# Kernel tuning notes

Hardware: AMD Instinct MI355X
Metric: run time of the kernel (lower is better)

## Reference

```python
import jax, jax.numpy as jnp
import numpy as np

B, S, D = 30, 1024, 128      # batch (hardcoded by module), seq_len, input_dim
ET, H, NH = 128, 4, 128      # embed_time, num_heads, nhidden
DK = ET // H


def setup_inputs() -> dict:
    key = jax.random.key(0)
    ks = jax.random.split(key, 32)
    s = 0.05
    p = lambda i, shape: jax.random.normal(ks[i], shape, jnp.float32) * s
    return dict(
        x=jax.random.normal(ks[0], (B, S, D), jnp.float32),
        time_steps=jax.random.uniform(ks[1], (B, S), jnp.float32),
        # learned time embedding: Linear(1,1) and Linear(1, ET-1)
        w_lin=p(2, (1, 1)), b_lin=p(3, (1,)),
        w_per=p(4, (ET - 1, 1)), b_per=p(5, (ET - 1,)),
        # attention projections
        Wq=p(6, (ET, ET)), bq=p(7, (ET,)),
        Wk=p(8, (ET, ET)), bk=p(9, (ET,)),
        Wo=p(10, (NH, D * H)), bo=p(11, (NH,)),
        # bidirectional GRU (forward / backward directions)
        Wih_f=p(12, (3 * NH, NH)), Whh_f=p(13, (3 * NH, NH)),
        bih_f=p(14, (3 * NH,)), bhh_f=p(15, (3 * NH,)),
        Wih_b=p(16, (3 * NH, NH)), Whh_b=p(17, (3 * NH, NH)),
        bih_b=p(18, (3 * NH,)), bhh_b=p(19, (3 * NH,)),
        # classifier (no activations in original Sequential)
        W1=p(20, (128, 2 * NH)), b1=p(21, (128,)),
        W2=p(22, (64, 128)), b2=p(23, (64,)),
        W3=p(24, (6, 64)), b3=p(25, (6,)),
    )


def _gru_final(xseq, Wih, Whh, bih, bhh):
    # xseq: [S, B, NH]; returns final hidden [B, NH] (PyTorch GRU equations)
    def step(h, xt):
        gi = xt @ Wih.T + bih
        gh = h @ Whh.T + bhh
        ir, iz, inn = jnp.split(gi, 3, axis=-1)
        hr, hz, hn = jnp.split(gh, 3, axis=-1)
        r = jax.nn.sigmoid(ir + hr)
        z = jax.nn.sigmoid(iz + hz)
        n = jnp.tanh(inn + r * hn)
        h_new = (1.0 - z) * n + z * h
        return h_new, None
    h0 = jnp.zeros((xseq.shape[1], Whh.shape[1]), xseq.dtype)
    hT, _ = jax.lax.scan(step, h0, xseq)
    return hT


def reference(x, time_steps, w_lin, b_lin, w_per, b_per, Wq, bq, Wk, bk, Wo, bo,
              Wih_f, Whh_f, bih_f, bhh_f, Wih_b, Whh_b, bih_b, bhh_b,
              W1, b1, W2, b2, W3, b3):
    # learned time embedding: cat([Linear(1,1)(t), sin(Linear(1,ET-1)(t))], -1)
    tt = time_steps[..., None]                                   # [B,S,1]
    te = jnp.concatenate([tt @ w_lin.T + b_lin,
                          jnp.sin(tt @ w_per.T + b_per)], -1)    # [B,S,ET]
    # q/k projections, split into heads
    q = (te @ Wq.T + bq).reshape(B, S, H, DK).transpose(0, 2, 1, 3)  # [B,H,S,DK]
    k = (te @ Wk.T + bk).reshape(B, S, H, DK).transpose(0, 2, 1, 3)
    scores = jnp.einsum('bhqd,bhkd->bhqk', q, k) / jnp.sqrt(jnp.float32(DK))
    # mask=None, dropout=None => the repeat_interleave over the feature dim is
    # redundant: softmax over the key axis is identical for every feature, so
    # sum(p_attn * value) == softmax(scores) @ value exactly.
    attn = jax.nn.softmax(scores, axis=-1)                       # [B,H,S,S]
    ctx = jnp.einsum('bhqk,bkd->bhqd', attn, x)                  # [B,H,S,D]
    att_out = ctx.transpose(0, 2, 1, 3).reshape(B, S, H * D) @ Wo.T + bo  # [B,S,NH]
    # bidirectional GRU; only final hidden states are used downstream
    xs = att_out.transpose(1, 0, 2)                              # [S,B,NH]
    hf = _gru_final(xs, Wih_f, Whh_f, bih_f, bhh_f)
    hb = _gru_final(xs[::-1], Wih_b, Whh_b, bih_b, bhh_b)
    cin = jnp.concatenate([hf, hb], axis=-1)                     # [B,2*NH]
    h1 = cin @ W1.T + b1
    h2 = h1 @ W2.T + b2
    return h2 @ W3.T + b3                                        # [B,6]
```

## Files before the change

### kernel.cpp

```cpp
#include <hip/hip_runtime.h>
#include <math.h>

#define B_ 30
#define S_ 1024
#define D_ 128
#define ET_ 128
#define H_ 4
#define DK_ 32
#define NH_ 128
#define NPOS (B_*S_)

#define OFF_TE   0L
#define OFF_Q    3932160L
#define OFF_K    7864320L
#define OFF_CTX  11796480L
#define OFF_XS   0L
#define OFF_GIF  3932160L
#define OFF_GIB  15728640L
#define OFF_HF   27525120L
#define OFF_HB   27528960L

typedef __attribute__((ext_vector_type(4))) short short4v;
typedef __attribute__((ext_vector_type(8))) short short8v;
typedef __attribute__((ext_vector_type(4))) float f32x4;

__device__ __forceinline__ short f2bf(float x) {
    unsigned u = __builtin_bit_cast(unsigned, x);
    unsigned r = (u + 0x7FFFu + ((u >> 16) & 1u)) >> 16;
    return (short)r;
}
__device__ __forceinline__ float bf2f(short s) {
    unsigned u = ((unsigned)(unsigned short)s) << 16;
    return __builtin_bit_cast(float, u);
}

__device__ __forceinline__ short8v pack8(const float4 a, const float4 b) {
    short8v v;
    v[0]=f2bf(a.x); v[1]=f2bf(a.y); v[2]=f2bf(a.z); v[3]=f2bf(a.w);
    v[4]=f2bf(b.x); v[5]=f2bf(b.y); v[6]=f2bf(b.z); v[7]=f2bf(b.w);
    return v;
}

__device__ __forceinline__ void pack_hilo(const float4 a, const float4 b,
                                          short8v& hi, short8v& lo) {
    float v[8] = {a.x,a.y,a.z,a.w,b.x,b.y,b.z,b.w};
#pragma unroll
    for (int e = 0; e < 8; ++e) {
        hi[e] = f2bf(v[e]);
        lo[e] = f2bf(v[e] - bf2f(hi[e]));
    }
}

__device__ __forceinline__ float fsigmoid(float x) {
    return __builtin_amdgcn_rcpf(1.f + __expf(-x));
}
__device__ __forceinline__ float ftanh(float x) {
    return 1.f - 2.f * __builtin_amdgcn_rcpf(__expf(2.f * x) + 1.f);
}

__device__ __forceinline__ void sync_lds() {
    asm volatile("s_waitcnt lgkmcnt(0)" ::: "memory");
    __builtin_amdgcn_sched_barrier(0);
    __builtin_amdgcn_s_barrier();
    __builtin_amdgcn_sched_barrier(0);
}

__global__ __launch_bounds__(256) void time_embed_kernel(
    const float* __restrict__ ts, const float* __restrict__ w_lin,
    const float* __restrict__ b_lin, const float* __restrict__ w_per,
    const float* __restrict__ b_per, float* __restrict__ te)
{
    const long idx = (long)blockIdx.x * 256 + threadIdx.x;
    const int pos = (int)(idx >> 7);
    const int j = (int)(idx & 127);
    const float tv = ts[pos];
    float v;
    if (j == 0) v = tv * w_lin[0] + b_lin[0];
    else        v = sinf(tv * w_per[j-1] + b_per[j-1]);
    te[idx] = v;
}

template<int REMAP, int FOLD>
__global__ __launch_bounds__(256) void gemm_mfma_kernel(
    const float* __restrict__ A, const float* __restrict__ W,
    const float* __restrict__ bias, const float* __restrict__ bias2,
    float* __restrict__ C, int M, int N, int K)
{
    __shared__ short A_hi[64][72], A_lo[64][72];
    __shared__ short W_hi[128][72], W_lo[128][72];
    const int t = threadIdx.x;
    const int m0 = blockIdx.x * 64;
    const int n0 = blockIdx.y * 128;
    const int w = t >> 6, lane = t & 63;
    const int l15 = lane & 15, lg = lane >> 4;

    f32x4 acc[8];
#pragma unroll
    for (int i = 0; i < 8; ++i) acc[i] = (f32x4){0.f,0.f,0.f,0.f};

    for (int k0 = 0; k0 < K; k0 += 64) {
        {
            const int r = t >> 2, c16 = (t & 3) * 16;
            const int m = m0 + r;
            long src;
            if (REMAP == 2) {
                const int s = m / B_, bb = m % B_;
                src = (long)((S_-1-s)*B_ + bb) * K;
            } else {
                src = (long)m * K;
            }
            const float4* ap = (const float4*)(A + src + k0 + c16);
            short8v h0, l0, h1, l1;
            pack_hilo(ap[0], ap[1], h0, l0);
            pack_hilo(ap[2], ap[3], h1, l1);
            *(short8v*)&A_hi[r][c16]     = h0;
            *(short8v*)&A_hi[r][c16 + 8] = h1;
            *(short8v*)&A_lo[r][c16]     = l0;
            *(short8v*)&A_lo[r][c16 + 8] = l1;
        }
        {
            const int n = t >> 1, c32 = (t & 1) * 32;
            const float4* wp = (const float4*)(W + (long)(n0 + n) * K + k0 + c32);
#pragma unroll
            for (int q = 0; q < 4; ++q) {
                short8v h, l;
                pack_hilo(wp[2*q], wp[2*q + 1], h, l);
                *(short8v*)&W_hi[n][c32 + 8*q] = h;
                *(short8v*)&W_lo[n][c32 + 8*q] = l;
            }
        }
        __syncthreads();
#pragma unroll
        for (int kk = 0; kk < 64; kk += 32) {
            short8v ah = *(const short8v*)&A_hi[16*w + l15][kk + 8*lg];
            short8v al = *(const short8v*)&A_lo[16*w + l15][kk + 8*lg];
#pragma unroll
            for (int nf = 0; nf < 8; ++nf) {
                short8v wh = *(const short8v*)&W_hi[16*nf + l15][kk + 8*lg];
                short8v wl = *(const short8v*)&W_lo[16*nf + l15][kk + 8*lg];
                acc[nf] = __builtin_amdgcn_mfma_f32_16x16x32_bf16(ah, wh, acc[nf], 0,0,0);
                acc[nf] = __builtin_amdgcn_mfma_f32_16x16x32_bf16(al, wh, acc[nf], 0,0,0);
                acc[nf] = __builtin_amdgcn_mfma_f32_16x16x32_bf16(ah, wl, acc[nf], 0,0,0);
            }
        }
        __syncthreads();
    }

#pragma unroll
    for (int nf = 0; nf < 8; ++nf) {
#pragma unroll
        for (int r = 0; r < 4; ++r) {
            const int n = n0 + 16*nf + l15;
            const int m = m0 + 16*w + 4*lg + r;
            float v = acc[nf][r] + bias[n];
            if (FOLD) { if (n < 256) v += bias2[n]; }
            if (REMAP == 1) {
                const int bb = m / S_, s = m % S_;
                C[(long)(s*B_ + bb) * N + n] = v;
            } else {
                C[(long)m * N + n] = v;
            }
        }
    }
}

#define SCALE_LOG2 (0.17677669529663687f * 1.4426950408889634f)

__global__ __launch_bounds__(256) void attn_kernel(
    const float* __restrict__ qbuf, const float* __restrict__ kbuf,
    const float* __restrict__ x, float* __restrict__ ctx)
{
    const int qt = blockIdx.x;
    const int h  = blockIdx.y;
    const int b  = blockIdx.z;
    const int q0 = qt * 64;
    const int t  = threadIdx.x;
    const int w    = t >> 6;
    const int lane = t & 63;
    const int l15  = lane & 15;
    const int lg   = lane >> 4;

    __shared__ short K_lds[64][40];
    __shared__ short XT_lds[128][68];
    __shared__ short P_lds[4][16][88];

    short8v qf;
    {
        const float* qp = qbuf + ((long)(b*S_ + q0 + 16*w + l15))*ET_ + h*DK_ + 8*lg;
        float4 a = *(const float4*)qp;
        float4 c = *(const float4*)(qp + 4);
        a.x*=SCALE_LOG2; a.y*=SCALE_LOG2; a.z*=SCALE_LOG2; a.w*=SCALE_LOG2;
        c.x*=SCALE_LOG2; c.y*=SCALE_LOG2; c.z*=SCALE_LOG2; c.w*=SCALE_LOG2;
        qf = pack8(a, c);
    }

    short8v ones;
#pragma unroll
    for (int i = 0; i < 8; ++i) ones[i] = (short)0x3F80;

    f32x4 acc[8];
#pragma unroll
    for (int i = 0; i < 8; ++i) acc[i] = (f32x4){0.f,0.f,0.f,0.f};
    float lsum = 0.f;
    const f32x4 zf = (f32x4){0.f,0.f,0.f,0.f};

    for (int kt = 0; kt < 16; ++kt) {
        const int key0 = kt * 64;
        {
            const int key = t >> 2, c8 = (t & 3) * 8;
            const float* kp = kbuf + ((long)(b*S_ + key0 + key))*ET_ + h*DK_ + c8;
            float4 a = *(const float4*)kp;
            float4 c = *(const float4*)(kp + 4);
            *(short8v*)&K_lds[key][c8] = pack8(a, c);
        }
        {
            const int k2 = t & 31;
            const int dg = t >> 5;
            const float* xp0 = x + ((long)(b*S_ + key0 + 2*k2))*D_ + 16*dg;
            const float* xp1 = xp0 + D_;
            float v0[16], v1[16];
#pragma unroll
            for (int j4 = 0; j4 < 4; ++j4) {
                float4 a = ((const float4*)xp0)[j4];
                float4 c = ((const float4*)xp1)[j4];
                v0[4*j4+0]=a.x; v0[4*j4+1]=a.y; v0[4*j4+2]=a.z; v0[4*j4+3]=a.w;
                v1[4*j4+0]=c.x; v1[4*j4+1]=c.y; v1[4*j4+2]=c.z; v1[4*j4+3]=c.w;
            }
#pragma unroll
            for (int j = 0; j < 16; ++j) {
                unsigned u = (unsigned)(unsigned short)f2bf(v0[j])
                           | ((unsigned)(unsigned short)f2bf(v1[j]) << 16);
                *(unsigned*)&XT_lds[16*dg + j][2*k2] = u;
            }
        }
        __syncthreads();

        f32x4 sc[4];
#pragma unroll
        for (int f = 0; f < 4; ++f) {
            short8v kf = *(const short8v*)&K_lds[16*f + l15][8*lg];
            sc[f] = __builtin_amdgcn_mfma_f32_16x16x32_bf16(kf, qf, zf, 0, 0, 0);
        }

        float pw[4][4];
        float ps = 0.f;
#pragma unroll
        for (int f = 0; f < 4; ++f)
#pragma unroll
            for (int r = 0; r < 4; ++r) {
                const float p = exp2f(sc[f][r]);
                ps += p;
                pw[f][r] = p - 1.f;
            }
        ps += __shfl_xor(ps, 16);
        ps += __shfl_xor(ps, 32);
        lsum += ps;

#pragma unroll
        for (int f = 0; f < 4; ++f) {
            unsigned lo = (unsigned)(unsigned short)f2bf(pw[f][0])
                        | ((unsigned)(unsigned short)f2bf(pw[f][1]) << 16);
            unsigned hi = (unsigned)(unsigned short)f2bf(pw[f][2])
                        | ((unsigned)(unsigned short)f2bf(pw[f][3]) << 16);
            *(unsigned*)&P_lds[w][l15][16*f + 4*lg]     = lo;
            *(unsigned*)&P_lds[w][l15][16*f + 4*lg + 2] = hi;
        }

#pragma unroll
        for (int kb = 0; kb < 2; ++kb) {
            short8v pa = *(const short8v*)&P_lds[w][l15][32*kb + 8*lg];
#pragma unroll
            for (int dq = 0; dq < 8; ++dq) {
                const short* xr = &XT_lds[16*dq + l15][32*kb + 8*lg];
                short4v lo = *(const short4v*)xr;
                short4v hi = *(const short4v*)(xr + 4);
                short8v xb = __builtin_shufflevector(lo, hi, 0,1,2,3,4,5,6,7);
                acc[dq] = __builtin_amdgcn_mfma_f32_16x16x32_bf16(ones, xb, acc[dq], 0, 0, 0);
                acc[dq] = __builtin_amdgcn_mfma_f32_16x16x32_bf16(pa,   xb, acc[dq], 0, 0, 0);
            }
        }
        __syncthreads();
    }

    const float inv = 1.f / lsum;
#pragma unroll
    for (int r = 0; r < 4; ++r) {
        const float ir = __shfl(inv, (lane & 48) | (4*lg + r));
        const long base = ((long)(b*S_ + q0 + 16*w + 4*lg + r)*H_ + h)*D_ + l15;
#pragma unroll
        for (int d = 0; d < 8; ++d)
            ctx[base + (long)d*16] = acc[d][r] * ir;
    }
}

__global__ __launch_bounds__(512, 1) void gru_kernel(
    const float* __restrict__ gi_f, const float* __restrict__ gi_b,
    const float* __restrict__ Whh_f, const float* __restrict__ bhh_f,
    const float* __restrict__ Whh_b, const float* __restrict__ bhh_b,
    float* __restrict__ hf, float* __restrict__ hb)
{
    const int bid = blockIdx.x;
    const int dir = bid / B_;
    const int b   = bid % B_;
    const float* gi  = dir ? gi_b  : gi_f;
    const float* Whh = dir ? Whh_b : Whh_f;
    const float* bhh = dir ? bhh_b : bhh_f;
    float* hout      = dir ? hb    : hf;
    const int t    = threadIdx.x;
    const int w    = t >> 6;
    const int lane = t & 63;
    const int l15  = lane & 15;
    const int lg   = lane >> 4;
    const int sel  = l15 >> 3;

    short8v wa[3][4];
#pragma unroll
    for (int rt = 0; rt < 3; ++rt) {
        const int row = (3*w + rt)*16 + l15;
#pragma unroll
        for (int kf = 0; kf < 4; ++kf) {
            const float* wp = Whh + (long)row*128 + 32*kf + 8*lg;
            float4 a = *(const float4*)wp;
            float4 c = *(const float4*)(wp + 4);
            wa[rt][kf] = pack8(a, c);
        }
    }

    __shared__ __align__(16) float ghs[800];
    __shared__ __align__(16) short hbf[2][2][160];

    float hreg = 0.f;
    float bnj = 0.f;
    float gar = 0.f, gaz = 0.f, gan = 0.f;
    float gbr = 0.f, gbz = 0.f, gbn = 0.f;
    float gcr = 0.f, gcz = 0.f, gcn = 0.f;
    float gdr = 0.f, gdz = 0.f, gdn = 0.f;
    if (t < 128) {
        hbf[0][0][t] = 0; hbf[0][1][t] = 0;
        bnj = bhh[256 + t];
        const float* g0 = gi + (long)b * 384;
        gar = g0[t]; gaz = g0[128+t]; gan = g0[256+t];
        const float* g1 = gi + ((long)B_ + b) * 384;
        gbr = g1[t]; gbz = g1[128+t]; gbn = g1[256+t];
    }
    __syncthreads();

#define LOADGI(R, Z, N, SS)                                                    \
    if (t < 128 && (SS) < S_) {                                                \
        const float* g = gi + ((long)(SS)*B_ + b) * 384;                       \
        R = g[t]; Z = g[128+t]; N = g[256+t];                                  \
    }

#define GRU_STEP(CUR, GR, GZ, GN)                                              \
    {                                                                          \
        short8v hfrag[4];                                                      \
        _Pragma("unroll")                                                      \
        for (int kf = 0; kf < 4; ++kf)                                         \
            hfrag[kf] = *(const short8v*)&hbf[CUR][sel][32*kf + 8*lg];         \
        _Pragma("unroll")                                                      \
        for (int rt = 0; rt < 3; ++rt) {                                       \
            f32x4 cacc = (f32x4){0.f,0.f,0.f,0.f};                             \
            _Pragma("unroll")                                                  \
            for (int kf = 0; kf < 4; ++kf)                                     \
                cacc = __builtin_amdgcn_mfma_f32_16x16x32_bf16(                \
                    wa[rt][kf], hfrag[kf], cacc, 0,0,0);                       \
            if (l15 == 0)                                                      \
                *(f32x4*)&ghs[(3*w + rt)*16 + 4*lg] = cacc;                    \
            else if (l15 == 8)                                                 \
                *(f32x4*)&ghs[400 + (3*w + rt)*16 + 4*lg] = cacc;              \
        }                                                                      \
        sync_lds();                                                            \
        if (t < 128) {                                                         \
            const float ghr = ghs[t]       + ghs[400+t];                       \
            const float ghz = ghs[128+t]   + ghs[528+t];                       \
            const float ghn = ghs[256+t]   + ghs[656+t];                       \
            const float r = fsigmoid(GR + ghr);                                \
            const float z = fsigmoid(GZ + ghz);                                \
            const float n = ftanh (GN + r * (ghn + bnj));                      \
            hreg = (1.f - z)*n + z*hreg;                                       \
            const short hi = f2bf(hreg);                                       \
            hbf[(CUR)^1][0][t] = hi;                                           \
            hbf[(CUR)^1][1][t] = f2bf(hreg - bf2f(hi));                        \
        }                                                                      \
        sync_lds();                                                            \
    }

    for (int s = 0; s < S_; s += 4) {
        LOADGI(gcr, gcz, gcn, s + 2)
        GRU_STEP(0, gar, gaz, gan)
        LOADGI(gdr, gdz, gdn, s + 3)
        GRU_STEP(1, gbr, gbz, gbn)
        LOADGI(gar, gaz, gan, s + 4)
        GRU_STEP(0, gcr, gcz, gcn)
        LOADGI(gbr, gbz, gbn, s + 5)
        GRU_STEP(1, gdr, gdz, gdn)
    }
#undef GRU_STEP
#undef LOADGI

    if (t < 128) hout[(long)b*128 + t] = hreg;
}

__global__ __launch_bounds__(128) void classifier_kernel(
    const float* __restrict__ hf, const float* __restrict__ hb,
    const float* __restrict__ W1, const float* __restrict__ b1,
    const float* __restrict__ W2, const float* __restrict__ b2,
    const float* __restrict__ W3, const float* __restrict__ b3,
    float* __restrict__ out)
{
    const int b = blockIdx.x;
    const int t = threadIdx.x;
    __shared__ float cin[256], a1[128], a2[64];
    cin[t]       = hf[(long)b*128 + t];
    cin[128 + t] = hb[(long)b*128 + t];
    __syncthreads();
    {
        float a = b1[t];
        for (int i = 0; i < 256; ++i) a = fmaf(W1[(long)t*256 + i], cin[i], a);
        a1[t] = a;
    }
    __syncthreads();
    if (t < 64) {
        float a = b2[t];
        for (int i = 0; i < 128; ++i) a = fmaf(W2[(long)t*128 + i], a1[i], a);
        a2[t] = a;
    }
    __syncthreads();
    if (t < 6) {
        float a = b3[t];
        for (int i = 0; i < 64; ++i) a = fmaf(W3[(long)t*64 + i], a2[i], a);
        out[(long)b*6 + t] = a;
    }
}

extern "C" void kernel_launch(void* const* d_in, const int* in_sizes, int n_in,
                              void* d_out, int out_size, void* d_ws, size_t ws_size,
                              hipStream_t stream)
{
    const float* x     = (const float*)d_in[0];
    const float* ts    = (const float*)d_in[1];
    const float* w_lin = (const float*)d_in[2];
    const float* b_lin = (const float*)d_in[3];
    const float* w_per = (const float*)d_in[4];
    const float* b_per = (const float*)d_in[5];
    const float* Wq    = (const float*)d_in[6];
    const float* bq    = (const float*)d_in[7];
    const float* Wk    = (const float*)d_in[8];
    const float* bk    = (const float*)d_in[9];
    const float* Wo    = (const float*)d_in[10];
    const float* bo    = (const float*)d_in[11];
    const float* Wih_f = (const float*)d_in[12];
    const float* Whh_f = (const float*)d_in[13];
    const float* bih_f = (const float*)d_in[14];
    const float* bhh_f = (const float*)d_in[15];
    const float* Wih_b = (const float*)d_in[16];
    const float* Whh_b = (const float*)d_in[17];
    const float* bih_b = (const float*)d_in[18];
    const float* bhh_b = (const float*)d_in[19];
    const float* W1    = (const float*)d_in[20];
    const float* b1    = (const float*)d_in[21];
    const float* W2    = (const float*)d_in[22];
    const float* b2    = (const float*)d_in[23];
    const float* W3    = (const float*)d_in[24];
    const float* b3    = (const float*)d_in[25];
    float* out = (float*)d_out;
    float* ws  = (float*)d_ws;

    float* te  = ws + OFF_TE;
    float* q   = ws + OFF_Q;
    float* k   = ws + OFF_K;
    float* ctx = ws + OFF_CTX;
    float* xs  = ws + OFF_XS;
    float* gif = ws + OFF_GIF;
    float* gib = ws + OFF_GIB;
    float* hf  = ws + OFF_HF;
    float* hb  = ws + OFF_HB;

    time_embed_kernel<<<NPOS*128/256, 256, 0, stream>>>(ts, w_lin, b_lin, w_per, b_per, te);
    gemm_mfma_kernel<0,0><<<dim3(NPOS/64, 1), 256, 0, stream>>>(te, Wq, bq, nullptr, q, NPOS, 128, 128);
    gemm_mfma_kernel<0,0><<<dim3(NPOS/64, 1), 256, 0, stream>>>(te, Wk, bk, nullptr, k, NPOS, 128, 128);
    attn_kernel<<<dim3(16, 4, 30), 256, 0, stream>>>(q, k, x, ctx);
    gemm_mfma_kernel<1,0><<<dim3(NPOS/64, 1), 256, 0, stream>>>(ctx, Wo, bo, nullptr, xs, NPOS, 128, 512);
    gemm_mfma_kernel<0,1><<<dim3(NPOS/64, 3), 256, 0, stream>>>(xs, Wih_f, bih_f, bhh_f, gif, NPOS, 384, 128);
    gemm_mfma_kernel<2,1><<<dim3(NPOS/64, 3), 256, 0, stream>>>(xs, Wih_b, bih_b, bhh_b, gib, NPOS, 384, 128);
    gru_kernel<<<60, 512, 0, stream>>>(gif, gib, Whh_f, bhh_f, Whh_b, bhh_b, hf, hb);
    classifier_kernel<<<30, 128, 0, stream>>>(hf, hb, W1, b1, W2, b2, W3, b3, out);
}
```

Before: 952.7 us.

## Restructure GRU recurrence to two waves with in-register gate extraction

```diff
diff --git a/kernel.cpp b/kernel.cpp
--- a/kernel.cpp
+++ b/kernel.cpp
@@ -293,7 +293,7 @@
     }
 }
 
-__global__ __launch_bounds__(512, 1) void gru_kernel(
+__global__ __launch_bounds__(128, 1) void gru_kernel(
     const float* __restrict__ gi_f, const float* __restrict__ gi_b,
     const float* __restrict__ Whh_f, const float* __restrict__ bhh_f,
     const float* __restrict__ Whh_b, const float* __restrict__ bhh_b,
@@ -307,48 +307,48 @@
     const float* bhh = dir ? bhh_b : bhh_f;
     float* hout      = dir ? hb    : hf;
     const int t    = threadIdx.x;
-    const int w    = t >> 6;
+    const int wv   = t >> 6;
     const int lane = t & 63;
     const int l15  = lane & 15;
     const int lg   = lane >> 4;
-    const int sel  = l15 >> 3;
-
-    short8v wa[3][4];
-#pragma unroll
-    for (int rt = 0; rt < 3; ++rt) {
-        const int row = (3*w + rt)*16 + l15;
-#pragma unroll
-        for (int kf = 0; kf < 4; ++kf) {
-            const float* wp = Whh + (long)row*128 + 32*kf + 8*lg;
-            float4 a = *(const float4*)wp;
-            float4 c = *(const float4*)(wp + 4);
-            wa[rt][kf] = pack8(a, c);
-        }
-    }
-
-    __shared__ __align__(16) float ghs[800];
-    __shared__ __align__(16) short hbf[2][2][160];
-
-    float hreg = 0.f;
-    float bnj = 0.f;
-    float gar = 0.f, gaz = 0.f, gan = 0.f;
-    float gbr = 0.f, gbz = 0.f, gbn = 0.f;
-    float gcr = 0.f, gcz = 0.f, gcn = 0.f;
-    float gdr = 0.f, gdz = 0.f, gdn = 0.f;
-    if (t < 128) {
-        hbf[0][0][t] = 0; hbf[0][1][t] = 0;
-        bnj = bhh[256 + t];
+    const int j    = 64*wv + 16*(l15 >> 2) + 4*lg + (l15 & 3);
+
+    short8v wa[3][4][4];
+#pragma unroll
+    for (int g = 0; g < 3; ++g)
+#pragma unroll
+        for (int A = 0; A < 4; ++A) {
+            const int row = 128*g + 64*wv + 16*A + l15;
+#pragma unroll
+            for (int kf = 0; kf < 4; ++kf) {
+                const float* wp = Whh + (long)row*128 + 32*kf + 8*lg;
+                float4 a = *(const float4*)wp;
+                float4 c = *(const float4*)(wp + 4);
+                wa[g][A][kf] = pack8(a, c);
+            }
+        }
+
+    const float bnj = bhh[256 + j];
+
+    __shared__ __align__(16) short hbf[2][128];
+    hbf[0][t] = 0;
+
+    float hcur = 0.f;
+
+    float gar=0.f, gaz=0.f, gan=0.f, gbr=0.f, gbz=0.f, gbn=0.f;
+    float gcr=0.f, gcz=0.f, gcn=0.f, gdr=0.f, gdz=0.f, gdn=0.f;
+    {
         const float* g0 = gi + (long)b * 384;
-        gar = g0[t]; gaz = g0[128+t]; gan = g0[256+t];
+        gar = g0[j]; gaz = g0[128+j]; gan = g0[256+j];
         const float* g1 = gi + ((long)B_ + b) * 384;
-        gbr = g1[t]; gbz = g1[128+t]; gbn = g1[256+t];
+        gbr = g1[j]; gbz = g1[128+j]; gbn = g1[256+j];
     }
     __syncthreads();
 
 #define LOADGI(R, Z, N, SS)                                                    \
-    if (t < 128 && (SS) < S_) {                                                \
+    if ((SS) < S_) {                                                           \
         const float* g = gi + ((long)(SS)*B_ + b) * 384;                       \
-        R = g[t]; Z = g[128+t]; N = g[256+t];                                  \
+        R = g[j]; Z = g[128+j]; N = g[256+j];                                  \
     }
 
 #define GRU_STEP(CUR, GR, GZ, GN)                                              \
@@ -356,32 +356,39 @@
         short8v hfrag[4];                                                      \
         _Pragma("unroll")                                                      \
         for (int kf = 0; kf < 4; ++kf)                                         \
-            hfrag[kf] = *(const short8v*)&hbf[CUR][sel][32*kf + 8*lg];         \
+            hfrag[kf] = *(const short8v*)&hbf[CUR][32*kf + 8*lg];              \
+        f32x4 acc[3][4];                                                       \
         _Pragma("unroll")                                                      \
-        for (int rt = 0; rt < 3; ++rt) {                                       \
-            f32x4 cacc = (f32x4){0.f,0.f,0.f,0.f};                             \
+        for (int g = 0; g < 3; ++g)                                            \
             _Pragma("unroll")                                                  \
-            for (int kf = 0; kf < 4; ++kf)                                     \
-                cacc = __builtin_amdgcn_mfma_f32_16x16x32_bf16(                \
-                    wa[rt][kf], hfrag[kf], cacc, 0,0,0);                       \
-            if (l15 == 0)                                                      \
-                *(f32x4*)&ghs[(3*w + rt)*16 + 4*lg] = cacc;                    \
-            else if (l15 == 8)                                                 \
-                *(f32x4*)&ghs[400 + (3*w + rt)*16 + 4*lg] = cacc;              \
-        }                                                                      \
-        sync_lds();                                                            \
-        if (t < 128) {                                                         \
-            const float ghr = ghs[t]       + ghs[400+t];                       \
-            const float ghz = ghs[128+t]   + ghs[528+t];                       \
-            const float ghn = ghs[256+t]   + ghs[656+t];                       \
-            const float r = fsigmoid(GR + ghr);                                \
-            const float z = fsigmoid(GZ + ghz);                                \
-            const float n = ftanh (GN + r * (ghn + bnj));                      \
-            hreg = (1.f - z)*n + z*hreg;                                       \
-            const short hi = f2bf(hreg);                                       \
-            hbf[(CUR)^1][0][t] = hi;                                           \
-            hbf[(CUR)^1][1][t] = f2bf(hreg - bf2f(hi));                        \
-        }                                                                      \
+            for (int A = 0; A < 4; ++A)                                        \
+                acc[g][A] = (f32x4){0.f,0.f,0.f,0.f};                          \
+        _Pragma("unroll")                                                      \
+        for (int kf = 0; kf < 4; ++kf)                                         \
+            _Pragma("unroll")                                                  \
+            for (int g = 0; g < 3; ++g)                                        \
+                _Pragma("unroll")                                              \
+                for (int A = 0; A < 4; ++A)                                    \
+                    acc[g][A] = __builtin_amdgcn_mfma_f32_16x16x32_bf16(       \
+                        wa[g][A][kf], hfrag[kf], acc[g][A], 0,0,0);            \
+        float ghr = acc[0][0][0];                                              \
+        float ghz = acc[1][0][0];                                              \
+        float ghn = acc[2][0][0];                                              \
+        _Pragma("unroll")                                                      \
+        for (int A = 0; A < 4; ++A)                                            \
+            _Pragma("unroll")                                                  \
+            for (int R = 0; R < 4; ++R) {                                      \
+                if (A == 0 && R == 0) continue;                                \
+                const bool c = (l15 == 4*A + R);                               \
+                ghr = c ? acc[0][A][R] : ghr;                                  \
+                ghz = c ? acc[1][A][R] : ghz;                                  \
+                ghn = c ? acc[2][A][R] : ghn;                                  \
+            }                                                                  \
+        const float r = fsigmoid(GR + ghr);                                    \
+        const float z = fsigmoid(GZ + ghz);                                    \
+        const float n = ftanh (GN + r * (ghn + bnj));                          \
+        hcur = (1.f - z)*n + z*hcur;                                           \
+        hbf[(CUR)^1][j] = f2bf(hcur);                                          \
         sync_lds();                                                            \
     }
 
@@ -398,7 +405,7 @@
 #undef GRU_STEP
 #undef LOADGI
 
-    if (t < 128) hout[(long)b*128 + t] = hreg;
+    hout[(long)b*128 + j] = hcur;
 }
 
 __global__ __launch_bounds__(128) void classifier_kernel(
@@ -483,6 +490,6 @@
     gemm_mfma_kernel<1,0><<<dim3(NPOS/64, 1), 256, 0, stream>>>(ctx, Wo, bo, nullptr, xs, NPOS, 128, 512);
     gemm_mfma_kernel<0,1><<<dim3(NPOS/64, 3), 256, 0, stream>>>(xs, Wih_f, bih_f, bhh_f, gif, NPOS, 384, 128);
     gemm_mfma_kernel<2,1><<<dim3(NPOS/64, 3), 256, 0, stream>>>(xs, Wih_b, bih_b, bhh_b, gib, NPOS, 384, 128);
-    gru_kernel<<<60, 512, 0, stream>>>(gif, gib, Whh_f, bhh_f, Whh_b, bhh_b, hf, hb);
+    gru_kernel<<<60, 128, 0, stream>>>(gif, gib, Whh_f, bhh_f, Whh_b, bhh_b, hf, hb);
     classifier_kernel<<<30, 128, 0, stream>>>(hf, hb, W1, b1, W2, b2, W3, b3, out);
 }
```

Result: faster. 878.1 us (-7.8%).
